# Kernel optimization log

Measured on AMD Instinct MI355X. Metric: run time of the kernel, lower is better.

Reference implementation:

```python
import jax, jax.numpy as jnp
import numpy as np

B, S, D, H = 2, 2048, 1024, 16
DK = D // H


def setup_inputs() -> dict:
    key = jax.random.key(0)
    ks = jax.random.split(key, 12)
    scale = 1.0 / np.sqrt(D)
    inp = {
        "q": jax.random.normal(ks[0], (B, S, D), jnp.float32),
        "k": jax.random.normal(ks[1], (B, S, D), jnp.float32),
        "v": jax.random.normal(ks[2], (B, S, D), jnp.float32),
        "mask": jax.random.randint(ks[3], (B, 1, S, S), 0, 2, jnp.int32),
        "w_q": jax.random.normal(ks[4], (D, D), jnp.float32) * scale,
        "b_q": jnp.zeros((D,), jnp.float32),
        "w_k": jax.random.normal(ks[5], (D, D), jnp.float32) * scale,
        "b_k": jnp.zeros((D,), jnp.float32),
        "w_v": jax.random.normal(ks[6], (D, D), jnp.float32) * scale,
        "b_v": jnp.zeros((D,), jnp.float32),
        "w_o": jax.random.normal(ks[7], (D, D), jnp.float32) * scale,
        "b_o": jnp.zeros((D,), jnp.float32),
    }
    return inp


def reference(q, k, v, mask, w_q, b_q, w_k, b_k, w_v, b_v, w_o, b_o):
    # linear projections (torch Linear: x @ W.T + b)
    qp = q @ w_q.T + b_q  # [B,S,D]
    kp = k @ w_k.T + b_k
    vp = v @ w_v.T + b_v
    # split heads -> [B,H,S,DK]
    qh = qp.reshape(B, S, H, DK).transpose(0, 2, 1, 3)
    kh = kp.reshape(B, S, H, DK).transpose(0, 2, 1, 3)
    vh = vp.reshape(B, S, H, DK).transpose(0, 2, 1, 3)
    # scaled dot-product attention
    scores = jnp.einsum("bhqd,bhkd->bhqk", qh, kh) / jnp.sqrt(jnp.float32(DK))
    scores = jnp.where(mask == 0, jnp.float32(-1e9), scores)
    attn = jax.nn.softmax(scores, axis=-1)
    ctx = jnp.einsum("bhqk,bhkd->bhqd", attn, vh)  # [B,H,S,DK]
    ctx = ctx.transpose(0, 2, 1, 3).reshape(B, S, D)
    return ctx @ w_o.T + b_o
```

## Files before the change

kernel.cpp:

```cpp
#include <hip/hip_runtime.h>
#include <hip/hip_bf16.h>
#include <cstdint>

#define DEVINL __device__ __forceinline__

using bfrag = __attribute__((ext_vector_type(8))) __bf16;
using f32x4 = __attribute__((ext_vector_type(4))) float;
using f32x16 = __attribute__((ext_vector_type(16))) float;
using u16x4 = __attribute__((ext_vector_type(4))) unsigned short;
using u16x8 = __attribute__((ext_vector_type(8))) unsigned short;
using u32x4 = __attribute__((ext_vector_type(4))) unsigned int;

static constexpr int S_ = 2048;
static constexpr int D_ = 1024;
static constexpr int MROWS = 4096;

DEVINL unsigned short f2bf(float f) {
  __hip_bfloat16 h = __float2bfloat16(f);
  union { __hip_bfloat16 h; unsigned short u; } cv; cv.h = h; return cv.u;
}

DEVINL float fexp2(float x) {
#if __has_builtin(__builtin_amdgcn_exp2f)
  return __builtin_amdgcn_exp2f(x);
#else
  return exp2f(x);
#endif
}

DEVINL unsigned cvtpk(float lo, float hi) {
  unsigned r;
  asm("v_cvt_pk_bf16_f32 %0, %1, %2" : "=v"(r) : "v"(lo), "v"(hi));
  return r;
}

DEVINL void plswap(unsigned& x, unsigned& y) {
#if __has_builtin(__builtin_amdgcn_permlane32_swap)
  auto r = __builtin_amdgcn_permlane32_swap(x, y, false, false);
  x = r[0]; y = r[1];
#else
  unsigned px = __shfl_xor(x, 32), py = __shfl_xor(y, 32);
  bool h = (threadIdx.x & 32) != 0;
  unsigned nx = h ? py : x;
  unsigned ny = h ? y : px;
  x = nx; y = ny;
#endif
}

DEVINL void async_copy16(void* lds, const void* g) {
  __builtin_amdgcn_global_load_lds(
      (const __attribute__((address_space(1))) unsigned int*)g,
      (__attribute__((address_space(3))) unsigned int*)lds, 16, 0, 0);
}

struct CvtW {
  const float* src[4];
  unsigned short* dst[4];
  const int* mask;
  unsigned long long* bits;
  int nmask;
};

__global__ __launch_bounds__(256) void cvt_w(CvtW a) {
  if (blockIdx.y == 4) {
    const int n = a.nmask;
    for (int i = blockIdx.x * 256 + threadIdx.x; i < n; i += gridDim.x * 256) {
      unsigned long long b = __ballot(a.mask[i] != 0);
      if ((threadIdx.x & 63) == 0) a.bits[i >> 6] = b;
    }
    return;
  }
  const float* __restrict__ in = a.src[blockIdx.y];
  unsigned short* __restrict__ out = a.dst[blockIdx.y];
  const int n4 = D_ * D_ / 4;
  for (int i = blockIdx.x * 256 + threadIdx.x; i < n4; i += gridDim.x * 256) {
    f32x4 v = ((const f32x4*)in)[i];
    u16x4 o;
    o[0] = f2bf(v[0]); o[1] = f2bf(v[1]); o[2] = f2bf(v[2]); o[3] = f2bf(v[3]);
    ((u16x4*)out)[i] = o;
  }
}

template <int OMODE, bool AF32>
DEVINL void gemm_body(const void* __restrict__ Ap, const unsigned short* __restrict__ W,
                      const float* __restrict__ bias, void* __restrict__ Cout,
                      int K, int N, float oscale,
                      unsigned short* As, unsigned short* Bs, int m0, int n0) {
  const int t = threadIdx.x;
  const int lane = t & 63, wave = t >> 6;
  const int wr = wave >> 1, wc = wave & 1;
  const int g = lane >> 4, q = lane & 15;

  f32x4 acc[4][4] = {};

  const int srow = t >> 3;
  const int scol = (t & 7) * 8;
  const size_t bbase = (size_t)(n0 + srow) * K + scol;
  char* AsB = (char*)As;
  char* BsB = (char*)Bs;

  for (int k0 = 0; k0 < K; k0 += 64) {
    __syncthreads();
#pragma unroll
    for (int c = 0; c < 4; ++c)
      async_copy16(BsB + c * 4096 + wave * 1024, W + bbase + (size_t)c * 32 * K + k0);
    if (AF32) {
      const float* Af = (const float*)Ap;
      f32x4 v0[4], v1[4];
#pragma unroll
      for (int i = 0; i < 4; ++i) {
        const float* src = Af + (size_t)(m0 + (t >> 3) + i * 32) * K + k0 + (t & 7) * 8;
        v0[i] = *reinterpret_cast<const f32x4*>(src);
        v1[i] = *reinterpret_cast<const f32x4*>(src + 4);
      }
#pragma unroll
      for (int i = 0; i < 4; ++i) {
        u16x8 o;
#pragma unroll
        for (int j = 0; j < 4; ++j) { o[j] = f2bf(v0[i][j]); o[4 + j] = f2bf(v1[i][j]); }
        *reinterpret_cast<u16x8*>(AsB + ((t >> 3) + i * 32) * 128 + (t & 7) * 16) = o;
      }
    } else {
      const unsigned short* Ab = (const unsigned short*)Ap;
#pragma unroll
      for (int c = 0; c < 4; ++c)
        async_copy16(AsB + c * 4096 + wave * 1024,
                     Ab + (size_t)(m0 + srow + c * 32) * K + scol + k0);
    }
    __syncthreads();
#pragma unroll
    for (int kk = 0; kk < 64; kk += 32) {
      bfrag af[4], bf[4];
#pragma unroll
      for (int i = 0; i < 4; ++i)
        af[i] = *reinterpret_cast<const bfrag*>(&As[(wr * 64 + i * 16 + q) * 64 + kk + g * 8]);
#pragma unroll
      for (int j = 0; j < 4; ++j)
        bf[j] = *reinterpret_cast<const bfrag*>(&Bs[(wc * 64 + j * 16 + q) * 64 + kk + g * 8]);
#pragma unroll
      for (int i = 0; i < 4; ++i)
#pragma unroll
        for (int j = 0; j < 4; ++j)
          acc[i][j] = __builtin_amdgcn_mfma_f32_16x16x32_bf16(af[i], bf[j], acc[i][j], 0, 0, 0);
    }
  }

  float bv[4];
#pragma unroll
  for (int j = 0; j < 4; ++j) bv[j] = bias[n0 + wc * 64 + j * 16 + q];
#pragma unroll
  for (int i = 0; i < 4; ++i)
#pragma unroll
    for (int j = 0; j < 4; ++j) {
      int rowb = m0 + wr * 64 + i * 16 + g * 4;
      int col = n0 + wc * 64 + j * 16 + q;
      if (OMODE == 2) {
        u16x4 o;
#pragma unroll
        for (int r = 0; r < 4; ++r) o[r] = f2bf(acc[i][j][r] + bv[j]);
        *reinterpret_cast<u16x4*>(&((unsigned short*)Cout)[(size_t)col * MROWS + rowb]) = o;
      } else {
#pragma unroll
        for (int r = 0; r < 4; ++r) {
          float val = (acc[i][j][r] + bv[j]) * oscale;
          if (OMODE == 1)
            ((float*)Cout)[(size_t)(rowb + r) * N + col] = val;
          else
            ((unsigned short*)Cout)[(size_t)(rowb + r) * N + col] = f2bf(val);
        }
      }
    }
}

__global__ __launch_bounds__(256, 2) void qkv_gemm(const float* __restrict__ Aq,
                                                   const float* __restrict__ Ak,
                                                   const float* __restrict__ Av,
                                                   const unsigned short* __restrict__ Wbase,
                                                   const float* __restrict__ b_q,
                                                   const float* __restrict__ b_k,
                                                   const float* __restrict__ b_v,
                                                   unsigned short* __restrict__ Qp,
                                                   unsigned short* __restrict__ Kp,
                                                   unsigned short* __restrict__ VpT) {
  __shared__ unsigned short As[128 * 64];
  __shared__ unsigned short Bs[128 * 64];
  const int lin = blockIdx.x + 8 * (blockIdx.y + 32 * blockIdx.z);
  const int tile = (lin & 7) * 96 + (lin >> 3);
  const int bx = tile & 7, by = (tile >> 3) & 31, z = tile >> 8;
  const unsigned short* W = Wbase + (size_t)z * D_ * D_;
  const int m0 = by * 128, n0 = bx * 128;
  if (z == 2) {
    gemm_body<2, true>(Av, W, b_v, VpT, D_, D_, 1.0f, As, Bs, m0, n0);
  } else if (z == 1) {
    gemm_body<0, true>(Ak, W, b_k, Kp, D_, D_, 1.0f, As, Bs, m0, n0);
  } else {
    gemm_body<0, true>(Aq, W, b_q, Qp, D_, D_, 0.125f * 1.44269504088896340736f, As, Bs, m0, n0);
  }
}

__global__ __launch_bounds__(256, 2) void out_gemm(const unsigned short* __restrict__ A,
                                                   const unsigned short* __restrict__ W,
                                                   const float* __restrict__ bias,
                                                   float* __restrict__ out) {
  __shared__ unsigned short As[128 * 64];
  __shared__ unsigned short Bs[128 * 64];
  const int lin = blockIdx.x + 8 * blockIdx.y;
  const int tile = (lin & 7) * 32 + (lin >> 3);
  const int bx = tile & 7, by = tile >> 3;
  gemm_body<1, false>(A, W, bias, out, D_, D_, 1.0f, As, Bs, by * 128, bx * 128);
}

__global__ __launch_bounds__(256, 2) void attn_kernel(const unsigned short* __restrict__ Qp,
                                                      const unsigned short* __restrict__ Kp,
                                                      const unsigned short* __restrict__ VpT,
                                                      const unsigned int* __restrict__ mbits32,
                                                      unsigned short* __restrict__ ctx) {
  __shared__ unsigned short Ks[2][128 * 64];
  __shared__ unsigned short Vt[2][64 * 128];

  const int t = threadIdx.x, lane = t & 63, wave = t >> 6;
  const int hi = lane >> 5, qh = lane & 31;
  const int id = blockIdx.x + 16 * (blockIdx.y + 16 * blockIdx.z);
  const int tile = (id & 7) * 64 + (id >> 3);
  const int qt = tile & 15, bh = tile >> 4;
  const int h = bh & 15, b = bh >> 4;
  const int q0 = qt * 128;
  const int qrow = q0 + wave * 32 + qh;

  const size_t qoff = ((size_t)b * S_ + qrow) * D_ + h * 64;
  bfrag qf[4];
#pragma unroll
  for (int ks = 0; ks < 4; ++ks)
    qf[ks] = *reinterpret_cast<const bfrag*>(&Qp[qoff + ks * 16 + hi * 8]);

  f32x16 acc_o[2] = {};
  f32x16 acc_l = {};

  u16x8 onesv;
#pragma unroll
  for (int j = 0; j < 8; ++j) onesv[j] = 0x3F80;
  const bfrag ones = __builtin_bit_cast(bfrag, onesv);

  const int krow = wave * 8 + (lane >> 3);
  const int ksc = ((lane & 7) ^ (lane >> 3)) * 8;
  const size_t kbase = (size_t)b * S_ * D_ + (size_t)h * 64;
  const int vrow = wave * 4 + (lane >> 4);
  const int vsc = ((lane & 15) ^ (vrow & 7)) * 8;
  const size_t vtrow0 = (size_t)h * 64;
  const size_t vtcol0 = (size_t)b * S_;

  char* KsB = (char*)&Ks[0][0];
  char* VtB = (char*)&Vt[0][0];
  const unsigned int* mrow = mbits32 + ((size_t)b * S_ + qrow) * (S_ / 32);
  const int swz = qh & 7;

  constexpr int NT = S_ / 128;

  auto stage = [&](int buf, int ti) {
#pragma unroll
    for (int c = 0; c < 4; ++c)
      async_copy16(KsB + buf * 16384 + c * 4096 + wave * 1024,
                   &Kp[kbase + (size_t)(ti * 128 + c * 32 + krow) * D_ + ksc]);
#pragma unroll
    for (int c = 0; c < 4; ++c)
      async_copy16(VtB + buf * 16384 + c * 4096 + wave * 1024,
                   &VpT[(vtrow0 + c * 16 + vrow) * MROWS + vtcol0 + ti * 128 + vsc]);
  };

  stage(0, 0);
  __syncthreads();

  auto tile_body = [&](int ti, int cur) {
    const int nxt = cur ^ 1;
    if (ti + 1 < NT) stage(nxt, ti + 1);
    u32x4 m4 = *reinterpret_cast<const u32x4*>(mrow + ti * 4);

    f32x16 sc[4];
    const f32x16 fz = {};
    __builtin_amdgcn_s_setprio(1);
#pragma unroll
    for (int kb = 0; kb < 4; ++kb) {
#pragma unroll
      for (int ks = 0; ks < 4; ++ks) {
        bfrag kf = *reinterpret_cast<const bfrag*>(
            KsB + cur * 16384 + (kb * 32 + qh) * 128 + ((((2 * ks + hi) ^ swz) & 7) << 4));
        sc[kb] = __builtin_amdgcn_mfma_f32_32x32x16_bf16(kf, qf[ks], ks == 0 ? fz : sc[kb], 0, 0, 0);
      }
    }
    __builtin_amdgcn_s_setprio(0);

    const int sh4 = 4 * hi;
#pragma unroll
    for (int kb = 0; kb < 4; ++kb) {
      unsigned w = m4[kb] >> sh4;
#pragma unroll
      for (int g2 = 0; g2 < 4; ++g2) {
        unsigned nib = (w >> (8 * g2)) & 0xFu;
#pragma unroll
        for (int r3 = 0; r3 < 4; ++r3) {
          float p = fexp2(sc[kb][g2 * 4 + r3]);
          sc[kb][g2 * 4 + r3] = (nib & (1u << r3)) ? p : 0.f;
        }
      }
    }

    bfrag pa[8];
#pragma unroll
    for (int ks = 0; ks < 8; ++ks) {
      const int o = ks * 8;
      unsigned a1 = cvtpk(sc[(o + 0) >> 4][(o + 0) & 15], sc[(o + 1) >> 4][(o + 1) & 15]);
      unsigned a2 = cvtpk(sc[(o + 2) >> 4][(o + 2) & 15], sc[(o + 3) >> 4][(o + 3) & 15]);
      unsigned b1 = cvtpk(sc[(o + 4) >> 4][(o + 4) & 15], sc[(o + 5) >> 4][(o + 5) & 15]);
      unsigned b2 = cvtpk(sc[(o + 6) >> 4][(o + 6) & 15], sc[(o + 7) >> 4][(o + 7) & 15]);
      plswap(a1, b1);
      plswap(a2, b2);
      u32x4 wv; wv[0] = a1; wv[1] = a2; wv[2] = b1; wv[3] = b2;
      pa[ks] = __builtin_bit_cast(bfrag, wv);
    }

    __builtin_amdgcn_s_setprio(1);
#pragma unroll
    for (int ks = 0; ks < 8; ++ks) {
      acc_l = __builtin_amdgcn_mfma_f32_32x32x16_bf16(ones, pa[ks], acc_l, 0, 0, 0);
#pragma unroll
      for (int dblk = 0; dblk < 2; ++dblk) {
        bfrag va = *reinterpret_cast<const bfrag*>(
            VtB + cur * 16384 + (dblk * 32 + qh) * 256 + ((((2 * ks + hi) ^ swz) & 15) << 4));
        acc_o[dblk] = __builtin_amdgcn_mfma_f32_32x32x16_bf16(va, pa[ks], acc_o[dblk], 0, 0, 0);
      }
    }
    __builtin_amdgcn_s_setprio(0);
    __syncthreads();
  };

#pragma unroll 1
  for (int ti = 0; ti < NT; ti += 2) {
    tile_body(ti, 0);
    tile_body(ti + 1, 1);
  }

  float inv = 1.f / acc_l[0];
#pragma unroll
  for (int dblk = 0; dblk < 2; ++dblk)
#pragma unroll
    for (int g2 = 0; g2 < 4; ++g2) {
      u16x4 o;
#pragma unroll
      for (int r3 = 0; r3 < 4; ++r3) o[r3] = f2bf(acc_o[dblk][g2 * 4 + r3] * inv);
      int d0 = dblk * 32 + 8 * g2 + 4 * hi;
      *reinterpret_cast<u16x4*>(&ctx[((size_t)b * S_ + qrow) * D_ + h * 64 + d0]) = o;
    }
}

extern "C" void kernel_launch(void* const* d_in, const int* in_sizes, int n_in,
                              void* d_out, int out_size, void* d_ws, size_t ws_size,
                              hipStream_t stream) {
  const float* q = (const float*)d_in[0];
  const float* k = (const float*)d_in[1];
  const float* v = (const float*)d_in[2];
  const int* mask = (const int*)d_in[3];
  const float* w_q = (const float*)d_in[4];
  const float* b_q = (const float*)d_in[5];
  const float* w_k = (const float*)d_in[6];
  const float* b_k = (const float*)d_in[7];
  const float* w_v = (const float*)d_in[8];
  const float* b_v = (const float*)d_in[9];
  const float* w_o = (const float*)d_in[10];
  const float* b_o = (const float*)d_in[11];
  float* out = (float*)d_out;

  char* ws = (char*)d_ws;
  const size_t SZ_IN = (size_t)MROWS * D_ * 2;
  const size_t SZ_W = (size_t)D_ * D_ * 2;
  unsigned short* wqb = (unsigned short*)(ws + 3 * SZ_IN);
  unsigned short* wob = (unsigned short*)(ws + 3 * SZ_IN + 3 * SZ_W);
  unsigned short* Qp = (unsigned short*)(ws + 3 * SZ_IN + 4 * SZ_W);
  unsigned short* ctx = (unsigned short*)(ws + 6 * SZ_IN + 4 * SZ_W);
  unsigned long long* mbits = (unsigned long long*)(ws + 7 * SZ_IN + 4 * SZ_W);
  unsigned short* wkb = wqb + D_ * D_;
  unsigned short* wvb = wkb + D_ * D_;
  unsigned short* Kp = Qp + MROWS * D_;
  unsigned short* VpT = Kp + MROWS * D_;

  CvtW cw;
  cw.src[0] = w_q; cw.dst[0] = wqb;
  cw.src[1] = w_k; cw.dst[1] = wkb;
  cw.src[2] = w_v; cw.dst[2] = wvb;
  cw.src[3] = w_o; cw.dst[3] = wob;
  cw.mask = mask; cw.bits = mbits; cw.nmask = 2 * S_ * S_;
  cvt_w<<<dim3(1024, 5), 256, 0, stream>>>(cw);

  qkv_gemm<<<dim3(D_ / 128, MROWS / 128, 3), 256, 0, stream>>>(q, k, v, wqb, b_q, b_k, b_v,
                                                               Qp, Kp, VpT);

  attn_kernel<<<dim3(S_ / 128, 16, 2), 256, 0, stream>>>(Qp, Kp, VpT,
                                                         (const unsigned int*)mbits, ctx);

  out_gemm<<<dim3(D_ / 128, MROWS / 128), 256, 0, stream>>>(ctx, wob, b_o, out);
}
```

Before: 136.2 us.

## Double-buffer GEMM LDS tiles with XOR swizzle to overlap loads and MFMA

Rewrites the shared GEMM body used by the QKV and output projections into a two-stage software pipeline. The next K-tile is fetched (async copy for weights and bf16 A, register prefetch for fp32 A) while the current tile is computed, which hides global-load latency behind MFMA work. It also applies an XOR swizzle to the LDS layout to cut bank conflicts on fragment reads. The cost is doubled LDS per block (64KB) and more live registers for the prefetched A values, which may limit occupancy to fewer than two blocks per CU.

```diff
diff --git a/kernel.cpp b/kernel.cpp
--- a/kernel.cpp
+++ b/kernel.cpp
@@ -82,67 +82,94 @@
 }
 
 template <int OMODE, bool AF32>
-DEVINL void gemm_body(const void* __restrict__ Ap, const unsigned short* __restrict__ W,
+DEVINL void gemm_pipe(const void* __restrict__ Ap, const unsigned short* __restrict__ W,
                       const float* __restrict__ bias, void* __restrict__ Cout,
-                      int K, int N, float oscale,
-                      unsigned short* As, unsigned short* Bs, int m0, int n0) {
+                      float oscale, unsigned short* AsBuf, unsigned short* BsBuf,
+                      int m0, int n0) {
+  constexpr int K = D_, N = D_, NK = K / 64;
   const int t = threadIdx.x;
   const int lane = t & 63, wave = t >> 6;
   const int wr = wave >> 1, wc = wave & 1;
   const int g = lane >> 4, q = lane & 15;
+  const int srow = t >> 3;
+  const int sg = t & 7;
+  const int swz = sg ^ (srow & 7);
+  char* AsB = (char*)AsBuf;
+  char* BsB = (char*)BsBuf;
+  const float* Af = (const float*)Ap;
+  const unsigned short* Ab = (const unsigned short*)Ap;
 
   f32x4 acc[4][4] = {};
-
-  const int srow = t >> 3;
-  const int scol = (t & 7) * 8;
-  const size_t bbase = (size_t)(n0 + srow) * K + scol;
-  char* AsB = (char*)As;
-  char* BsB = (char*)Bs;
-
-  for (int k0 = 0; k0 < K; k0 += 64) {
-    __syncthreads();
+  f32x4 a0[4], a1[4];
+
+  auto stageW = [&](int buf, int k0) {
 #pragma unroll
     for (int c = 0; c < 4; ++c)
-      async_copy16(BsB + c * 4096 + wave * 1024, W + bbase + (size_t)c * 32 * K + k0);
-    if (AF32) {
-      const float* Af = (const float*)Ap;
-      f32x4 v0[4], v1[4];
-#pragma unroll
-      for (int i = 0; i < 4; ++i) {
-        const float* src = Af + (size_t)(m0 + (t >> 3) + i * 32) * K + k0 + (t & 7) * 8;
-        v0[i] = *reinterpret_cast<const f32x4*>(src);
-        v1[i] = *reinterpret_cast<const f32x4*>(src + 4);
-      }
-#pragma unroll
-      for (int i = 0; i < 4; ++i) {
-        u16x8 o;
-#pragma unroll
-        for (int j = 0; j < 4; ++j) { o[j] = f2bf(v0[i][j]); o[4 + j] = f2bf(v1[i][j]); }
-        *reinterpret_cast<u16x8*>(AsB + ((t >> 3) + i * 32) * 128 + (t & 7) * 16) = o;
-      }
-    } else {
-      const unsigned short* Ab = (const unsigned short*)Ap;
-#pragma unroll
-      for (int c = 0; c < 4; ++c)
-        async_copy16(AsB + c * 4096 + wave * 1024,
-                     Ab + (size_t)(m0 + srow + c * 32) * K + scol + k0);
-    }
-    __syncthreads();
+      async_copy16(BsB + buf * 16384 + c * 4096 + wave * 1024,
+                   W + (size_t)(n0 + c * 32 + srow) * K + k0 + swz * 8);
+  };
+  auto stageA_lds = [&](int buf, int k0) {
+#pragma unroll
+    for (int c = 0; c < 4; ++c)
+      async_copy16(AsB + buf * 16384 + c * 4096 + wave * 1024,
+                   Ab + (size_t)(m0 + c * 32 + srow) * K + k0 + swz * 8);
+  };
+  auto loadA = [&](int k0) {
+#pragma unroll
+    for (int i = 0; i < 4; ++i) {
+      const float* src = Af + (size_t)(m0 + srow + 32 * i) * K + k0 + sg * 8;
+      a0[i] = *reinterpret_cast<const f32x4*>(src);
+      a1[i] = *reinterpret_cast<const f32x4*>(src + 4);
+    }
+  };
+  auto writeA = [&](int buf) {
+#pragma unroll
+    for (int i = 0; i < 4; ++i) {
+      u16x8 o;
+#pragma unroll
+      for (int j = 0; j < 4; ++j) { o[j] = f2bf(a0[i][j]); o[4 + j] = f2bf(a1[i][j]); }
+      *reinterpret_cast<u16x8*>(AsB + buf * 16384 + (srow + 32 * i) * 128 + swz * 16) = o;
+    }
+  };
+  auto compute = [&](int cur) {
 #pragma unroll
     for (int kk = 0; kk < 64; kk += 32) {
+      const int gb = kk >> 3;
       bfrag af[4], bf[4];
 #pragma unroll
       for (int i = 0; i < 4; ++i)
-        af[i] = *reinterpret_cast<const bfrag*>(&As[(wr * 64 + i * 16 + q) * 64 + kk + g * 8]);
+        af[i] = *reinterpret_cast<const bfrag*>(
+            AsB + cur * 16384 + (wr * 64 + i * 16 + q) * 128 + (((gb + g) ^ (q & 7)) << 4));
 #pragma unroll
       for (int j = 0; j < 4; ++j)
-        bf[j] = *reinterpret_cast<const bfrag*>(&Bs[(wc * 64 + j * 16 + q) * 64 + kk + g * 8]);
+        bf[j] = *reinterpret_cast<const bfrag*>(
+            BsB + cur * 16384 + (wc * 64 + j * 16 + q) * 128 + (((gb + g) ^ (q & 7)) << 4));
 #pragma unroll
       for (int i = 0; i < 4; ++i)
 #pragma unroll
         for (int j = 0; j < 4; ++j)
           acc[i][j] = __builtin_amdgcn_mfma_f32_16x16x32_bf16(af[i], bf[j], acc[i][j], 0, 0, 0);
     }
+  };
+
+  stageW(0, 0);
+  if (AF32) { loadA(0); writeA(0); } else stageA_lds(0, 0);
+  __syncthreads();
+
+#pragma unroll 1
+  for (int ki = 0; ki < NK; ki += 2) {
+    stageW(1, (ki + 1) * 64);
+    if (AF32) loadA((ki + 1) * 64); else stageA_lds(1, (ki + 1) * 64);
+    compute(0);
+    if (AF32) writeA(1);
+    __syncthreads();
+    if (ki + 2 < NK) {
+      stageW(0, (ki + 2) * 64);
+      if (AF32) loadA((ki + 2) * 64); else stageA_lds(0, (ki + 2) * 64);
+    }
+    compute(1);
+    if (AF32 && ki + 2 < NK) writeA(0);
+    __syncthreads();
   }
 
   float bv[4];
@@ -182,19 +209,19 @@
                                                    unsigned short* __restrict__ Qp,
                                                    unsigned short* __restrict__ Kp,
                                                    unsigned short* __restrict__ VpT) {
-  __shared__ unsigned short As[128 * 64];
-  __shared__ unsigned short Bs[128 * 64];
+  __shared__ unsigned short As[2 * 128 * 64];
+  __shared__ unsigned short Bs[2 * 128 * 64];
   const int lin = blockIdx.x + 8 * (blockIdx.y + 32 * blockIdx.z);
   const int tile = (lin & 7) * 96 + (lin >> 3);
   const int bx = tile & 7, by = (tile >> 3) & 31, z = tile >> 8;
   const unsigned short* W = Wbase + (size_t)z * D_ * D_;
   const int m0 = by * 128, n0 = bx * 128;
   if (z == 2) {
-    gemm_body<2, true>(Av, W, b_v, VpT, D_, D_, 1.0f, As, Bs, m0, n0);
+    gemm_pipe<2, true>(Av, W, b_v, VpT, 1.0f, As, Bs, m0, n0);
   } else if (z == 1) {
-    gemm_body<0, true>(Ak, W, b_k, Kp, D_, D_, 1.0f, As, Bs, m0, n0);
+    gemm_pipe<0, true>(Ak, W, b_k, Kp, 1.0f, As, Bs, m0, n0);
   } else {
-    gemm_body<0, true>(Aq, W, b_q, Qp, D_, D_, 0.125f * 1.44269504088896340736f, As, Bs, m0, n0);
+    gemm_pipe<0, true>(Aq, W, b_q, Qp, 0.125f * 1.44269504088896340736f, As, Bs, m0, n0);
   }
 }
 
@@ -202,12 +229,12 @@
                                                    const unsigned short* __restrict__ W,
                                                    const float* __restrict__ bias,
                                                    float* __restrict__ out) {
-  __shared__ unsigned short As[128 * 64];
-  __shared__ unsigned short Bs[128 * 64];
+  __shared__ unsigned short As[2 * 128 * 64];
+  __shared__ unsigned short Bs[2 * 128 * 64];
   const int lin = blockIdx.x + 8 * blockIdx.y;
   const int tile = (lin & 7) * 32 + (lin >> 3);
   const int bx = tile & 7, by = tile >> 3;
-  gemm_body<1, false>(A, W, bias, out, D_, D_, 1.0f, As, Bs, by * 128, bx * 128);
+  gemm_pipe<1, false>(A, W, bias, out, 1.0f, As, Bs, by * 128, bx * 128);
 }
 
 __global__ __launch_bounds__(256, 2) void attn_kernel(const unsigned short* __restrict__ Qp,
```

Result: faster. 130.3 us (-4.4%).

## Async-copy fp32 A tiles to LDS with XOR swizzle, convert at fragment load

Applied to the files above, without the earlier changes.

The QKV GEMM now streams fp32 activation tiles straight into shared memory with async copies instead of loading them through registers, converting to bf16 and storing. The bf16 conversion moves to the point where MFMA fragments are read from LDS. An XOR swizzle is applied to both A and B tile layouts to reduce LDS bank conflicts. This doubles the LDS footprint of the A tile and repeats the conversion work per wave, which may lower occupancy.

```diff
diff --git a/kernel.cpp b/kernel.cpp
--- a/kernel.cpp
+++ b/kernel.cpp
@@ -84,8 +84,8 @@
 template <int OMODE, bool AF32>
 DEVINL void gemm_body(const void* __restrict__ Ap, const unsigned short* __restrict__ W,
                       const float* __restrict__ bias, void* __restrict__ Cout,
-                      int K, int N, float oscale,
-                      unsigned short* As, unsigned short* Bs, int m0, int n0) {
+                      float oscale, char* AsB, char* BsB, int m0, int n0) {
+  constexpr int K = D_, N = D_;
   const int t = threadIdx.x;
   const int lane = t & 63, wave = t >> 6;
   const int wr = wave >> 1, wc = wave & 1;
@@ -94,49 +94,56 @@
   f32x4 acc[4][4] = {};
 
   const int srow = t >> 3;
-  const int scol = (t & 7) * 8;
-  const size_t bbase = (size_t)(n0 + srow) * K + scol;
-  char* AsB = (char*)As;
-  char* BsB = (char*)Bs;
+  const int sgz = (t & 7) ^ (srow & 7);
+  const int arow = ((t >> 6) & 3) * 4 + ((t >> 4) & 3);
+  const int agz = ((t & 15) ^ ((((t >> 6) & 1) << 2) | ((t >> 4) & 3))) * 4;
+  const float* Af = (const float*)Ap;
+  const unsigned short* Ab = (const unsigned short*)Ap;
 
   for (int k0 = 0; k0 < K; k0 += 64) {
     __syncthreads();
 #pragma unroll
     for (int c = 0; c < 4; ++c)
-      async_copy16(BsB + c * 4096 + wave * 1024, W + bbase + (size_t)c * 32 * K + k0);
+      async_copy16(BsB + c * 4096 + wave * 1024,
+                   W + (size_t)(n0 + c * 32 + srow) * K + k0 + sgz * 8);
     if (AF32) {
-      const float* Af = (const float*)Ap;
-      f32x4 v0[4], v1[4];
-#pragma unroll
-      for (int i = 0; i < 4; ++i) {
-        const float* src = Af + (size_t)(m0 + (t >> 3) + i * 32) * K + k0 + (t & 7) * 8;
-        v0[i] = *reinterpret_cast<const f32x4*>(src);
-        v1[i] = *reinterpret_cast<const f32x4*>(src + 4);
-      }
-#pragma unroll
-      for (int i = 0; i < 4; ++i) {
-        u16x8 o;
-#pragma unroll
-        for (int j = 0; j < 4; ++j) { o[j] = f2bf(v0[i][j]); o[4 + j] = f2bf(v1[i][j]); }
-        *reinterpret_cast<u16x8*>(AsB + ((t >> 3) + i * 32) * 128 + (t & 7) * 16) = o;
-      }
+#pragma unroll
+      for (int c = 0; c < 8; ++c)
+        async_copy16(AsB + c * 4096 + wave * 1024,
+                     Af + (size_t)(m0 + c * 16 + arow) * K + k0 + agz);
     } else {
-      const unsigned short* Ab = (const unsigned short*)Ap;
 #pragma unroll
       for (int c = 0; c < 4; ++c)
         async_copy16(AsB + c * 4096 + wave * 1024,
-                     Ab + (size_t)(m0 + srow + c * 32) * K + scol + k0);
+                     Ab + (size_t)(m0 + c * 32 + srow) * K + k0 + sgz * 8);
     }
     __syncthreads();
 #pragma unroll
     for (int kk = 0; kk < 64; kk += 32) {
       bfrag af[4], bf[4];
 #pragma unroll
-      for (int i = 0; i < 4; ++i)
-        af[i] = *reinterpret_cast<const bfrag*>(&As[(wr * 64 + i * 16 + q) * 64 + kk + g * 8]);
-#pragma unroll
-      for (int j = 0; j < 4; ++j)
-        bf[j] = *reinterpret_cast<const bfrag*>(&Bs[(wc * 64 + j * 16 + q) * 64 + kk + g * 8]);
+      for (int i = 0; i < 4; ++i) {
+        const int ar = wr * 64 + i * 16 + q;
+        if (AF32) {
+          const char* Ar = AsB + ar * 256;
+          const int gi = (kk >> 2) + 2 * g;
+          f32x4 v0 = *reinterpret_cast<const f32x4*>(Ar + ((gi ^ (q & 7)) << 4));
+          f32x4 v1 = *reinterpret_cast<const f32x4*>(Ar + (((gi + 1) ^ (q & 7)) << 4));
+          u32x4 wv;
+          wv[0] = cvtpk(v0[0], v0[1]); wv[1] = cvtpk(v0[2], v0[3]);
+          wv[2] = cvtpk(v1[0], v1[1]); wv[3] = cvtpk(v1[2], v1[3]);
+          af[i] = __builtin_bit_cast(bfrag, wv);
+        } else {
+          af[i] = *reinterpret_cast<const bfrag*>(
+              AsB + ar * 128 + ((((kk >> 3) + g) ^ (q & 7)) << 4));
+        }
+      }
+#pragma unroll
+      for (int j = 0; j < 4; ++j) {
+        const int br = wc * 64 + j * 16 + q;
+        bf[j] = *reinterpret_cast<const bfrag*>(
+            BsB + br * 128 + ((((kk >> 3) + g) ^ (q & 7)) << 4));
+      }
 #pragma unroll
       for (int i = 0; i < 4; ++i)
 #pragma unroll
@@ -182,19 +189,19 @@
                                                    unsigned short* __restrict__ Qp,
                                                    unsigned short* __restrict__ Kp,
                                                    unsigned short* __restrict__ VpT) {
-  __shared__ unsigned short As[128 * 64];
-  __shared__ unsigned short Bs[128 * 64];
+  __shared__ char As[128 * 64 * 4];
+  __shared__ char Bs[128 * 64 * 2];
   const int lin = blockIdx.x + 8 * (blockIdx.y + 32 * blockIdx.z);
   const int tile = (lin & 7) * 96 + (lin >> 3);
   const int bx = tile & 7, by = (tile >> 3) & 31, z = tile >> 8;
   const unsigned short* W = Wbase + (size_t)z * D_ * D_;
   const int m0 = by * 128, n0 = bx * 128;
   if (z == 2) {
-    gemm_body<2, true>(Av, W, b_v, VpT, D_, D_, 1.0f, As, Bs, m0, n0);
+    gemm_body<2, true>(Av, W, b_v, VpT, 1.0f, As, Bs, m0, n0);
   } else if (z == 1) {
-    gemm_body<0, true>(Ak, W, b_k, Kp, D_, D_, 1.0f, As, Bs, m0, n0);
+    gemm_body<0, true>(Ak, W, b_k, Kp, 1.0f, As, Bs, m0, n0);
   } else {
-    gemm_body<0, true>(Aq, W, b_q, Qp, D_, D_, 0.125f * 1.44269504088896340736f, As, Bs, m0, n0);
+    gemm_body<0, true>(Aq, W, b_q, Qp, 0.125f * 1.44269504088896340736f, As, Bs, m0, n0);
   }
 }
 
@@ -202,12 +209,12 @@
                                                    const unsigned short* __restrict__ W,
                                                    const float* __restrict__ bias,
                                                    float* __restrict__ out) {
-  __shared__ unsigned short As[128 * 64];
-  __shared__ unsigned short Bs[128 * 64];
+  __shared__ char As[128 * 64 * 2];
+  __shared__ char Bs[128 * 64 * 2];
   const int lin = blockIdx.x + 8 * blockIdx.y;
   const int tile = (lin & 7) * 32 + (lin >> 3);
   const int bx = tile & 7, by = tile >> 3;
-  gemm_body<1, false>(A, W, bias, out, D_, D_, 1.0f, As, Bs, by * 128, bx * 128);
+  gemm_body<1, false>(A, W, bias, out, 1.0f, As, Bs, by * 128, bx * 128);
 }
 
 __global__ __launch_bounds__(256, 2) void attn_kernel(const unsigned short* __restrict__ Qp,
```

Measured after the change: 127.6 us. 6.3% less time.
